# Kernel optimization log

Measured on AMD Instinct MI355X. Metric: run time of the kernel, lower is better.

## Reference

```python
import jax, jax.numpy as jnp
import numpy as np

N = 3072      # packed vision tokens (multiple of _BLOCK=128, so no padding needed)
D = 1280      # hidden_size
H = 16        # num_heads
K = 80        # head_dim = D // H
NSEG = 8      # number of packed images/segments


def setup_inputs() -> dict:
    key = jax.random.key(0)
    ks = jax.random.split(key, 8)
    hidden_ND = jax.random.normal(ks[0], (N, D), jnp.float32)
    inner = jnp.sort(jax.random.randint(ks[1], (NSEG - 1,), 1, N)).astype(jnp.int32)
    cu_seqlens = jnp.concatenate([
        jnp.zeros((1,), jnp.int32), inner, jnp.full((1,), N, jnp.int32)])
    theta = jax.random.uniform(ks[2], (N, K), jnp.float32, 0.0, 2.0 * np.pi)
    cos_NK = jnp.cos(theta)
    sin_NK = jnp.sin(theta)
    sd = 1.0 / np.sqrt(D)  # lecun_normal-ish scale
    qkv_w = jax.random.normal(ks[3], (D, 3 * D), jnp.float32) * sd
    qkv_b = jax.random.normal(ks[4], (3 * D,), jnp.float32) * 0.01
    proj_w = jax.random.normal(ks[5], (D, D), jnp.float32) * sd
    proj_b = jax.random.normal(ks[6], (D,), jnp.float32) * 0.01
    return {"hidden_ND": hidden_ND, "cu_seqlens": cu_seqlens,
            "cos_NK": cos_NK, "sin_NK": sin_NK,
            "qkv_w": qkv_w, "qkv_b": qkv_b,
            "proj_w": proj_w, "proj_b": proj_b}


def _rotate_half(x):
    x1, x2 = jnp.split(x, 2, axis=-1)
    return jnp.concatenate([-x2, x1], axis=-1)


def _apply_vision_rope(q_NHK, k_NHK, cos_NK, sin_NK):
    c = cos_NK[:, None, :]  # (N, 1, K) broadcast over heads
    s = sin_NK[:, None, :]
    q = q_NHK * c + _rotate_half(q_NHK) * s
    k = k_NHK * c + _rotate_half(k_NHK) * s
    return q, k


def reference(hidden_ND, cu_seqlens, cos_NK, sin_NK, qkv_w, qkv_b, proj_w, proj_b):
    n = hidden_ND.shape[0]
    scale = K ** (-0.5)
    qkv = (hidden_ND @ qkv_w + qkv_b).reshape(n, 3, H, K)
    q_NHK, k_NHK, v_NHK = qkv[:, 0], qkv[:, 1], qkv[:, 2]
    q_NHK, k_NHK = _apply_vision_rope(q_NHK, k_NHK, cos_NK, sin_NK)

    # segment-boundary mask: token i attends to [k_start[i], k_end[i])
    idx = jnp.arange(n)
    seg = jnp.searchsorted(cu_seqlens[1:], idx, side='right')
    nseg = cu_seqlens.shape[0]
    k_start = cu_seqlens[jnp.minimum(seg, nseg - 2)]
    k_end = cu_seqlens[jnp.minimum(seg + 1, nseg - 1)]
    mask = (idx[None, :] >= k_start[:, None]) & (idx[None, :] < k_end[:, None])  # (Nq, Nk)

    scores = jnp.einsum('nhk,mhk->hnm', q_NHK, k_NHK) * scale  # (H, N, N)
    scores = jnp.where(mask[None], scores, jnp.float32(-1e30))
    probs = jax.nn.softmax(scores, axis=-1)
    attn = jnp.einsum('hnm,mhk->nhk', probs, v_NHK)  # (N, H, K)
    out_ND = attn.reshape(n, H * K) @ proj_w + proj_b
    return out_ND
```

## Files before the change

kernel.cpp:

```cpp
#include <hip/hip_runtime.h>

#define NTOK 3072
#define DM   1280
#define NH   16
#define HD   80
#define HDS  104
#define KVB  64
#define NSEG 8
#define QKVC 3840

typedef __attribute__((ext_vector_type(4))) float  f32x4;
typedef __attribute__((ext_vector_type(8))) __bf16 bf16x8;
typedef __attribute__((ext_vector_type(8))) unsigned short ushort8;
typedef __attribute__((ext_vector_type(4))) unsigned short ushort4v;

static __device__ __forceinline__ unsigned short f2bf(float f){
  union{float f; unsigned int u;} v; v.f=f;
  unsigned int r = v.u + 0x7fffu + ((v.u>>16)&1u);
  return (unsigned short)(r>>16);
}
static __device__ __forceinline__ float bf2f(unsigned short u){
  union{unsigned int i; float f;} v; v.i = ((unsigned int)u)<<16; return v.f;
}
static __device__ __forceinline__ void gload_lds16(const void* g, void* l){
  __builtin_amdgcn_global_load_lds((const __attribute__((address_space(1))) void*)g,
                                   (__attribute__((address_space(3))) void*)l, 16, 0, 0);
}

__global__ void cast_f32_bf16(const float* __restrict__ src, unsigned short* __restrict__ dst, int n){
  int i = (blockIdx.x*256 + threadIdx.x)*4;
  if (i >= n) return;
  f32x4 v = *reinterpret_cast<const f32x4*>(&src[i]);
  ushort4v o;
  o[0]=f2bf(v[0]); o[1]=f2bf(v[1]); o[2]=f2bf(v[2]); o[3]=f2bf(v[3]);
  *reinterpret_cast<ushort4v*>(&dst[i]) = o;
}

__global__ void transpose_cast(const float* __restrict__ src, unsigned short* __restrict__ dst, int R, int C){
  __shared__ unsigned short tile[32][33];
  int c0 = blockIdx.x*32, r0 = blockIdx.y*32;
  int tx = threadIdx.x, ty = threadIdx.y;
  #pragma unroll
  for (int i=0;i<4;i++){
    int r = r0 + ty + i*8;
    tile[ty+i*8][tx] = f2bf(src[(size_t)r*C + c0 + tx]);
  }
  __syncthreads();
  #pragma unroll
  for (int i=0;i<4;i++){
    int c = c0 + ty + i*8;
    dst[(size_t)c*R + r0 + tx] = tile[tx][ty+i*8];
  }
}

__global__ void transpose_v(const unsigned short* __restrict__ qkv, unsigned short* __restrict__ Vt){
  __shared__ unsigned short tile[32][33];
  int n0 = blockIdx.x*32, d0 = blockIdx.y*32, h = blockIdx.z;
  int tx = threadIdx.x, ty = threadIdx.y;
  #pragma unroll
  for (int i=0;i<4;i++){
    int n = n0 + ty + i*8;
    int d = d0 + tx;
    tile[ty+i*8][tx] = (d < HD) ? qkv[(size_t)n*QKVC + 2*DM + h*HD + d] : (unsigned short)0;
  }
  __syncthreads();
  #pragma unroll
  for (int i=0;i<4;i++){
    int d = d0 + ty + i*8;
    if (d < HD) Vt[((size_t)h*HD + d)*NTOK + n0 + tx] = tile[tx][ty+i*8];
  }
}

template<int OUT_BF16>
__global__ __launch_bounds__(256) void gemm_bt(
    const unsigned short* __restrict__ A,
    const unsigned short* __restrict__ Bt,
    const float* __restrict__ bias,
    unsigned short* __restrict__ Cb,
    float* __restrict__ Cf,
    int M, int Ncol, int Kd)
{
  __shared__ unsigned short As[2][128*32];
  __shared__ unsigned short Bs[2][128*32];
  const int tid  = threadIdx.x;
  const int lane = tid & 63, wave = tid >> 6;
  const int wr = wave >> 1, wc = wave & 1;
  const int bm = blockIdx.y, bn = blockIdx.x;
  const f32x4 vzero = {0.f,0.f,0.f,0.f};

  f32x4 acc[4][4];
  #pragma unroll
  for (int i=0;i<4;i++)
    #pragma unroll
    for (int j=0;j<4;j++) acc[i][j] = vzero;

  const int rsub = lane>>2;
  const int kc   = (lane&3)*8;
  const unsigned short* Ab = A  + (size_t)(bm*128 + wave*32 + rsub)*Kd + kc;
  const unsigned short* Bb = Bt + (size_t)(bn*128 + wave*32 + rsub)*Kd + kc;

  #pragma unroll
  for (int i=0;i<2;i++){
    gload_lds16(Ab + (size_t)i*16*Kd, &As[0][(wave*2+i)*512]);
    gload_lds16(Bb + (size_t)i*16*Kd, &Bs[0][(wave*2+i)*512]);
  }
  __syncthreads();

  int cur = 0;
  for (int k0=32; k0<Kd; k0+=32){
    #pragma unroll
    for (int i=0;i<2;i++){
      gload_lds16(Ab + (size_t)i*16*Kd + k0, &As[cur^1][(wave*2+i)*512]);
      gload_lds16(Bb + (size_t)i*16*Kd + k0, &Bs[cur^1][(wave*2+i)*512]);
    }
    bf16x8 a[4], b[4];
    #pragma unroll
    for (int mf=0; mf<4; mf++)
      a[mf] = *reinterpret_cast<const bf16x8*>(&As[cur][(wr*64 + mf*16 + (lane&15))*32 + ((lane>>4)<<3)]);
    #pragma unroll
    for (int nf=0; nf<4; nf++)
      b[nf] = *reinterpret_cast<const bf16x8*>(&Bs[cur][(wc*64 + nf*16 + (lane&15))*32 + ((lane>>4)<<3)]);
    #pragma unroll
    for (int mf=0; mf<4; mf++)
      #pragma unroll
      for (int nf=0; nf<4; nf++)
        acc[mf][nf] = __builtin_amdgcn_mfma_f32_16x16x32_bf16(a[mf], b[nf], acc[mf][nf], 0,0,0);
    __syncthreads();
    cur ^= 1;
  }
  {
    bf16x8 a[4], b[4];
    #pragma unroll
    for (int mf=0; mf<4; mf++)
      a[mf] = *reinterpret_cast<const bf16x8*>(&As[cur][(wr*64 + mf*16 + (lane&15))*32 + ((lane>>4)<<3)]);
    #pragma unroll
    for (int nf=0; nf<4; nf++)
      b[nf] = *reinterpret_cast<const bf16x8*>(&Bs[cur][(wc*64 + nf*16 + (lane&15))*32 + ((lane>>4)<<3)]);
    #pragma unroll
    for (int mf=0; mf<4; mf++)
      #pragma unroll
      for (int nf=0; nf<4; nf++)
        acc[mf][nf] = __builtin_amdgcn_mfma_f32_16x16x32_bf16(a[mf], b[nf], acc[mf][nf], 0,0,0);
  }

  const int crow0 = bm*128 + wr*64;
  const int ccol0 = bn*128 + wc*64;
  #pragma unroll
  for (int nf=0; nf<4; nf++){
    int col = ccol0 + nf*16 + (lane&15);
    float bv = bias[col];
    #pragma unroll
    for (int mf=0; mf<4; mf++){
      #pragma unroll
      for (int r=0;r<4;r++){
        int row = crow0 + mf*16 + ((lane>>4)<<2) + r;
        float v = acc[mf][nf][r] + bv;
        if (OUT_BF16) Cb[(size_t)row*Ncol + col] = f2bf(v);
        else          Cf[(size_t)row*Ncol + col] = v;
      }
    }
  }
}

__global__ void rope_repack(const unsigned short* __restrict__ qkv,
                            const float* __restrict__ cosNK, const float* __restrict__ sinNK,
                            unsigned short* __restrict__ Qr, unsigned short* __restrict__ Kr)
{
  int idx = blockIdx.x*256 + threadIdx.x;
  if (idx >= NH*NTOK*HDS) return;
  int k  = idx % HDS;
  int nh = idx / HDS;
  int n  = nh % NTOK;
  int h  = nh / NTOK;
  size_t dsti = (size_t)(h*NTOK + n)*HDS + k;
  if (k >= HD){ Qr[dsti]=0; Kr[dsti]=0; return; }
  float c = cosNK[n*HD + k], s = sinNK[n*HD + k];
  int   kp  = (k < 40) ? (k+40) : (k-40);
  float sgn = (k < 40) ? -1.f : 1.f;
  size_t base = (size_t)n*QKVC + h*HD;
  float q   = bf2f(qkv[base + k]);
  float qp  = bf2f(qkv[base + kp]);
  float kk  = bf2f(qkv[base + DM + k]);
  float kkp = bf2f(qkv[base + DM + kp]);
  Qr[dsti] = f2bf(q*c  + sgn*qp*s);
  Kr[dsti] = f2bf(kk*c + sgn*kkp*s);
}

__global__ __launch_bounds__(256) void attn_kernel(
    const unsigned short* __restrict__ Qr,
    const unsigned short* __restrict__ Kr,
    const unsigned short* __restrict__ Vt,
    const int* __restrict__ cu,
    unsigned short* __restrict__ attn_out)
{
  __shared__ unsigned short Qs[64*HDS];
  __shared__ unsigned short Ks[2][KVB*HDS];
  __shared__ unsigned short Ps[64*KVB];
  __shared__ int rs[64], re[64];

  const int h   = blockIdx.y;
  const int q0  = blockIdx.x*64;
  const int tid = threadIdx.x;
  const int lane = tid & 63, wave = tid >> 6;
  const int l16 = lane & 15, g16 = lane >> 4;
  const f32x4 vzero = {0.f,0.f,0.f,0.f};

  if (tid < 64){
    int row = q0 + tid, seg = 0;
    #pragma unroll
    for (int j=1;j<NSEG;j++) seg += (cu[j] <= row) ? 1 : 0;
    rs[tid] = cu[seg]; re[tid] = cu[seg+1];
  }
  int seg0 = 0, seg1 = 0;
  #pragma unroll
  for (int j=1;j<NSEG;j++){
    seg0 += (cu[j] <= q0) ? 1 : 0;
    seg1 += (cu[j] <= q0+63) ? 1 : 0;
  }
  const int kmin = cu[seg0], kmax = cu[seg1+1];
  const int kt0 = kmin & ~(KVB-1);
  const int nt  = (kmax - kt0 + KVB-1)/KVB;

  {
    const char* src = (const char*)(Qr + (size_t)(h*NTOK + q0)*HDS);
    #pragma unroll
    for (int i=0;i<4;i++){
      int t = tid + i*256;
      if (t < 832) gload_lds16(src + (size_t)t*16, (char*)Qs + (size_t)t*16);
    }
  }
  {
    const char* src = (const char*)(Kr + (size_t)(h*NTOK + kt0)*HDS);
    #pragma unroll
    for (int i=0;i<4;i++){
      int t = tid + i*256;
      if (t < 832) gload_lds16(src + (size_t)t*16, (char*)Ks[0] + (size_t)t*16);
    }
  }
  __syncthreads();

  f32x4 accO[5];
  #pragma unroll
  for (int i=0;i<5;i++) accO[i] = vzero;
  float m_r[4] = {-1e30f,-1e30f,-1e30f,-1e30f};
  float l_r[4] = {0.f,0.f,0.f,0.f};
  const float scale = 0.11180339887498948f;

  int cur = 0;
  for (int it = 0; it < nt; ++it){
    const int kt  = kt0 + it*KVB;
    const int ktn = kt0 + ((it+1 < nt) ? (it+1) : (nt-1))*KVB;
    {
      const char* src = (const char*)(Kr + (size_t)(h*NTOK + ktn)*HDS);
      #pragma unroll
      for (int i=0;i<4;i++){
        int t = tid + i*256;
        if (t < 832) gload_lds16(src + (size_t)t*16, (char*)Ks[cur^1] + (size_t)t*16);
      }
    }
    ushort8 vreg[2][5];
    #pragma unroll
    for (int ks=0; ks<2; ks++)
      #pragma unroll
      for (int cf=0; cf<5; cf++)
        vreg[ks][cf] = *reinterpret_cast<const ushort8*>(
            &Vt[((size_t)h*HD + cf*16 + l16)*NTOK + kt + ks*32 + g16*8]);

    f32x4 accS[4];
    #pragma unroll
    for (int i=0;i<4;i++) accS[i] = vzero;
    #pragma unroll
    for (int ks=0; ks<3; ks++){
      bf16x8 aq = *reinterpret_cast<const bf16x8*>((const char*)Qs + (wave*16 + l16)*208 + ks*64 + g16*16);
      #pragma unroll
      for (int nf=0;nf<4;nf++){
        bf16x8 bk = *reinterpret_cast<const bf16x8*>((const char*)Ks[cur] + (nf*16 + l16)*208 + ks*64 + g16*16);
        accS[nf] = __builtin_amdgcn_mfma_f32_16x16x32_bf16(aq, bk, accS[nf], 0,0,0);
      }
    }
    #pragma unroll
    for (int r=0;r<4;r++){
      const int row_i = wave*16 + g16*4 + r;
      const int rst = rs[row_i], ren = re[row_i];
      float sv[4]; bool ok[4];
      float mx = -1e30f;
      #pragma unroll
      for (int nf=0;nf<4;nf++){
        int kcol = kt + nf*16 + l16;
        ok[nf] = (kcol >= rst) && (kcol < ren);
        sv[nf] = accS[nf][r]*scale;
        if (ok[nf]) mx = fmaxf(mx, sv[nf]);
      }
      #pragma unroll
      for (int d=1; d<16; d<<=1) mx = fmaxf(mx, __shfl_xor(mx, d, 64));
      float mnew  = fmaxf(m_r[r], mx);
      float alpha = __expf(m_r[r] - mnew);
      m_r[r] = mnew;
      float lsum = 0.f;
      #pragma unroll
      for (int nf=0;nf<4;nf++){
        float p = ok[nf] ? __expf(sv[nf] - mnew) : 0.f;
        int pb = (row_i*128 + nf*32 + l16*2) ^ ((row_i&7)<<4);
        *reinterpret_cast<unsigned short*>((char*)Ps + pb) = f2bf(p);
        lsum += p;
      }
      #pragma unroll
      for (int d=1; d<16; d<<=1) lsum += __shfl_xor(lsum, d, 64);
      l_r[r] = l_r[r]*alpha + lsum;
      #pragma unroll
      for (int cf=0; cf<5; cf++) accO[cf][r] *= alpha;
    }
    #pragma unroll
    for (int ks=0; ks<2; ks++){
      const int arow = wave*16 + l16;
      bf16x8 ap = *reinterpret_cast<const bf16x8*>((char*)Ps + ((arow*128 + ks*64 + g16*16) ^ ((arow&7)<<4)));
      #pragma unroll
      for (int cf=0; cf<5; cf++){
        bf16x8 bv = __builtin_bit_cast(bf16x8, vreg[ks][cf]);
        accO[cf] = __builtin_amdgcn_mfma_f32_16x16x32_bf16(ap, bv, accO[cf], 0,0,0);
      }
    }
    __syncthreads();
    cur ^= 1;
  }

  #pragma unroll
  for (int cf=0; cf<5; cf++){
    #pragma unroll
    for (int r=0;r<4;r++){
      int row = q0 + wave*16 + g16*4 + r;
      int col = h*HD + cf*16 + l16;
      attn_out[(size_t)row*DM + col] = f2bf(accO[cf][r] / l_r[r]);
    }
  }
}

extern "C" void kernel_launch(void* const* d_in, const int* in_sizes, int n_in,
                              void* d_out, int out_size, void* d_ws, size_t ws_size,
                              hipStream_t stream)
{
  const float* hidden = (const float*)d_in[0];
  const int*   cu     = (const int*)  d_in[1];
  const float* cosNK  = (const float*)d_in[2];
  const float* sinNK  = (const float*)d_in[3];
  const float* qkv_w  = (const float*)d_in[4];
  const float* qkv_b  = (const float*)d_in[5];
  const float* proj_w = (const float*)d_in[6];
  const float* proj_b = (const float*)d_in[7];
  float* out = (float*)d_out;

  char* w = (char*)d_ws;
  unsigned short* hid_bf  = (unsigned short*)w;  w += (size_t)NTOK*DM*2;
  unsigned short* qkvwT   = (unsigned short*)w;  w += (size_t)QKVC*DM*2;
  unsigned short* projwT  = (unsigned short*)w;  w += (size_t)DM*DM*2;
  unsigned short* qkv_bf  = (unsigned short*)w;  w += (size_t)NTOK*QKVC*2;
  unsigned short* Qr      = (unsigned short*)w;  w += (size_t)NH*NTOK*HDS*2;
  unsigned short* Kr      = (unsigned short*)w;  w += (size_t)NH*NTOK*HDS*2;
  unsigned short* Vt      = qkvwT;
  unsigned short* attn_bf = hid_bf;

  cast_f32_bf16<<<(NTOK*DM/4 + 255)/256, 256, 0, stream>>>(hidden, hid_bf, NTOK*DM);
  transpose_cast<<<dim3(QKVC/32, DM/32), dim3(32,8), 0, stream>>>(qkv_w, qkvwT, DM, QKVC);
  transpose_cast<<<dim3(DM/32,  DM/32), dim3(32,8), 0, stream>>>(proj_w, projwT, DM, DM);
  gemm_bt<1><<<dim3(QKVC/128, NTOK/128), 256, 0, stream>>>(hid_bf, qkvwT, qkv_b, qkv_bf, nullptr, NTOK, QKVC, DM);
  rope_repack<<<(NH*NTOK*HDS + 255)/256, 256, 0, stream>>>(qkv_bf, cosNK, sinNK, Qr, Kr);
  transpose_v<<<dim3(NTOK/32, 3, NH), dim3(32,8), 0, stream>>>(qkv_bf, Vt);
  attn_kernel<<<dim3(NTOK/64, NH), 256, 0, stream>>>(Qr, Kr, Vt, cu, attn_bf);
  gemm_bt<0><<<dim3(DM/128, NTOK/128), 256, 0, stream>>>(attn_bf, projwT, proj_b, nullptr, out, NTOK, DM, DM);
}
```

Baseline: 268.2 us.

## Compute transposed S in attention with Q in registers; remap GEMM blocks across XCDs

The attention kernel now computes S transposed (K·Q^T), so each lane owns one query row. Q stays in registers, K is read straight from global memory instead of being staged in LDS, and the per-row max and sum reductions drop to two shuffles. This removes the LDS staging and the __syncthreads barrier, and lets the output be written as vector stores. Both GEMMs switch to a 1-D grid whose block ids are remapped by id mod 8, intended to give each XCD a contiguous group of output tiles for better L2 reuse; the cost is that K loads no longer go through LDS and get no reuse there.

```diff
diff --git a/kernel.cpp b/kernel.cpp
--- a/kernel.cpp
+++ b/kernel.cpp
@@ -13,6 +13,7 @@
 typedef __attribute__((ext_vector_type(8))) __bf16 bf16x8;
 typedef __attribute__((ext_vector_type(8))) unsigned short ushort8;
 typedef __attribute__((ext_vector_type(4))) unsigned short ushort4v;
+typedef __attribute__((ext_vector_type(2))) unsigned int  u32x2;
 
 static __device__ __forceinline__ unsigned short f2bf(float f){
   union{float f; unsigned int u;} v; v.f=f;
@@ -78,14 +79,16 @@
     const float* __restrict__ bias,
     unsigned short* __restrict__ Cb,
     float* __restrict__ Cf,
-    int M, int Ncol, int Kd)
+    int M, int Ncol, int Kd, int nbn)
 {
   __shared__ unsigned short As[2][128*32];
   __shared__ unsigned short Bs[2][128*32];
   const int tid  = threadIdx.x;
   const int lane = tid & 63, wave = tid >> 6;
   const int wr = wave >> 1, wc = wave & 1;
-  const int bm = blockIdx.y, bn = blockIdx.x;
+  const int cpx = gridDim.x >> 3;
+  const int id  = (blockIdx.x & 7)*cpx + (blockIdx.x >> 3);
+  const int bm = id / nbn, bn = id % nbn;
   const f32x4 vzero = {0.f,0.f,0.f,0.f};
 
   f32x4 acc[4][4];
@@ -193,71 +196,47 @@
     const int* __restrict__ cu,
     unsigned short* __restrict__ attn_out)
 {
-  __shared__ unsigned short Qs[64*HDS];
-  __shared__ unsigned short Ks[2][KVB*HDS];
   __shared__ unsigned short Ps[64*KVB];
-  __shared__ int rs[64], re[64];
 
   const int h   = blockIdx.y;
   const int q0  = blockIdx.x*64;
   const int tid = threadIdx.x;
   const int lane = tid & 63, wave = tid >> 6;
   const int l16 = lane & 15, g16 = lane >> 4;
+  const int qrow = q0 + wave*16 + l16;
   const f32x4 vzero = {0.f,0.f,0.f,0.f};
 
-  if (tid < 64){
-    int row = q0 + tid, seg = 0;
-    #pragma unroll
-    for (int j=1;j<NSEG;j++) seg += (cu[j] <= row) ? 1 : 0;
-    rs[tid] = cu[seg]; re[tid] = cu[seg+1];
-  }
-  int seg0 = 0, seg1 = 0;
+  int seg = 0, seg0 = 0, seg1 = 0;
   #pragma unroll
   for (int j=1;j<NSEG;j++){
-    seg0 += (cu[j] <= q0) ? 1 : 0;
-    seg1 += (cu[j] <= q0+63) ? 1 : 0;
-  }
+    int c = cu[j];
+    seg  += (c <= qrow)  ? 1 : 0;
+    seg0 += (c <= q0)    ? 1 : 0;
+    seg1 += (c <= q0+63) ? 1 : 0;
+  }
+  const int rst = cu[seg], ren = cu[seg+1];
   const int kmin = cu[seg0], kmax = cu[seg1+1];
   const int kt0 = kmin & ~(KVB-1);
-  const int nt  = (kmax - kt0 + KVB-1)/KVB;
-
+
+  bf16x8 bq[3];
   {
-    const char* src = (const char*)(Qr + (size_t)(h*NTOK + q0)*HDS);
-    #pragma unroll
-    for (int i=0;i<4;i++){
-      int t = tid + i*256;
-      if (t < 832) gload_lds16(src + (size_t)t*16, (char*)Qs + (size_t)t*16);
-    }
-  }
-  {
-    const char* src = (const char*)(Kr + (size_t)(h*NTOK + kt0)*HDS);
-    #pragma unroll
-    for (int i=0;i<4;i++){
-      int t = tid + i*256;
-      if (t < 832) gload_lds16(src + (size_t)t*16, (char*)Ks[0] + (size_t)t*16);
-    }
-  }
-  __syncthreads();
+    const unsigned short* qsrc = Qr + ((size_t)h*NTOK + qrow)*HDS;
+    #pragma unroll
+    for (int ds=0; ds<3; ds++)
+      bq[ds] = *reinterpret_cast<const bf16x8*>(&qsrc[ds*32 + g16*8]);
+  }
 
   f32x4 accO[5];
   #pragma unroll
   for (int i=0;i<5;i++) accO[i] = vzero;
-  float m_r[4] = {-1e30f,-1e30f,-1e30f,-1e30f};
-  float l_r[4] = {0.f,0.f,0.f,0.f};
+  float m_r = -1e30f, l_r = 0.f;
   const float scale = 0.11180339887498948f;
 
-  int cur = 0;
-  for (int it = 0; it < nt; ++it){
-    const int kt  = kt0 + it*KVB;
-    const int ktn = kt0 + ((it+1 < nt) ? (it+1) : (nt-1))*KVB;
-    {
-      const char* src = (const char*)(Kr + (size_t)(h*NTOK + ktn)*HDS);
-      #pragma unroll
-      for (int i=0;i<4;i++){
-        int t = tid + i*256;
-        if (t < 832) gload_lds16(src + (size_t)t*16, (char*)Ks[cur^1] + (size_t)t*16);
-      }
-    }
+  const int prow  = wave*16 + l16;
+  char* const psb = (char*)Ps;
+  const int pswz  = (prow & 7) << 4;
+
+  for (int kt = kt0; kt < kmax; kt += KVB){
     ushort8 vreg[2][5];
     #pragma unroll
     for (int ks=0; ks<2; ks++)
@@ -266,72 +245,78 @@
         vreg[ks][cf] = *reinterpret_cast<const ushort8*>(
             &Vt[((size_t)h*HD + cf*16 + l16)*NTOK + kt + ks*32 + g16*8]);
 
-    f32x4 accS[4];
-    #pragma unroll
-    for (int i=0;i<4;i++) accS[i] = vzero;
-    #pragma unroll
-    for (int ks=0; ks<3; ks++){
-      bf16x8 aq = *reinterpret_cast<const bf16x8*>((const char*)Qs + (wave*16 + l16)*208 + ks*64 + g16*16);
-      #pragma unroll
-      for (int nf=0;nf<4;nf++){
-        bf16x8 bk = *reinterpret_cast<const bf16x8*>((const char*)Ks[cur] + (nf*16 + l16)*208 + ks*64 + g16*16);
-        accS[nf] = __builtin_amdgcn_mfma_f32_16x16x32_bf16(aq, bk, accS[nf], 0,0,0);
-      }
-    }
-    #pragma unroll
-    for (int r=0;r<4;r++){
-      const int row_i = wave*16 + g16*4 + r;
-      const int rst = rs[row_i], ren = re[row_i];
-      float sv[4]; bool ok[4];
-      float mx = -1e30f;
-      #pragma unroll
-      for (int nf=0;nf<4;nf++){
-        int kcol = kt + nf*16 + l16;
-        ok[nf] = (kcol >= rst) && (kcol < ren);
-        sv[nf] = accS[nf][r]*scale;
-        if (ok[nf]) mx = fmaxf(mx, sv[nf]);
-      }
-      #pragma unroll
-      for (int d=1; d<16; d<<=1) mx = fmaxf(mx, __shfl_xor(mx, d, 64));
-      float mnew  = fmaxf(m_r[r], mx);
-      float alpha = __expf(m_r[r] - mnew);
-      m_r[r] = mnew;
-      float lsum = 0.f;
-      #pragma unroll
-      for (int nf=0;nf<4;nf++){
-        float p = ok[nf] ? __expf(sv[nf] - mnew) : 0.f;
-        int pb = (row_i*128 + nf*32 + l16*2) ^ ((row_i&7)<<4);
-        *reinterpret_cast<unsigned short*>((char*)Ps + pb) = f2bf(p);
-        lsum += p;
-      }
-      #pragma unroll
-      for (int d=1; d<16; d<<=1) lsum += __shfl_xor(lsum, d, 64);
-      l_r[r] = l_r[r]*alpha + lsum;
-      #pragma unroll
-      for (int cf=0; cf<5; cf++) accO[cf][r] *= alpha;
-    }
+    const unsigned short* ksrc = Kr + ((size_t)h*NTOK + kt)*HDS;
+    f32x4 accST[4];
+    #pragma unroll
+    for (int i=0;i<4;i++) accST[i] = vzero;
+    #pragma unroll
+    for (int ds=0; ds<3; ds++){
+      #pragma unroll
+      for (int f=0; f<4; f++){
+        bf16x8 ak = *reinterpret_cast<const bf16x8*>(&ksrc[(size_t)(f*16 + l16)*HDS + ds*32 + g16*8]);
+        accST[f] = __builtin_amdgcn_mfma_f32_16x16x32_bf16(ak, bq[ds], accST[f], 0,0,0);
+      }
+    }
+
+    float mx = -1e30f;
+    #pragma unroll
+    for (int f=0; f<4; f++){
+      #pragma unroll
+      for (int r=0; r<4; r++){
+        int kcol = kt + f*16 + g16*4 + r;
+        bool ok = (kcol >= rst) && (kcol < ren);
+        float s = accST[f][r]*scale;
+        accST[f][r] = ok ? s : -3e38f;
+        mx = fmaxf(mx, accST[f][r]);
+      }
+    }
+    mx = fmaxf(mx, __shfl_xor(mx, 16));
+    mx = fmaxf(mx, __shfl_xor(mx, 32));
+    const float mnew  = fmaxf(m_r, mx);
+    const float alpha = __expf(m_r - mnew);
+    m_r = mnew;
+    float lsum = 0.f;
+    #pragma unroll
+    for (int f=0; f<4; f++){
+      #pragma unroll
+      for (int r=0; r<4; r++){
+        float e = __expf(accST[f][r] - mnew);
+        accST[f][r] = e;
+        lsum += e;
+      }
+    }
+    lsum += __shfl_xor(lsum, 16);
+    lsum += __shfl_xor(lsum, 32);
+    l_r = l_r*alpha + lsum;
+    #pragma unroll
+    for (int cf=0; cf<5; cf++) accO[cf] *= alpha;
+
+    #pragma unroll
+    for (int f=0; f<4; f++){
+      u32x2 pk;
+      pk[0] = (unsigned int)f2bf(accST[f][0]) | ((unsigned int)f2bf(accST[f][1]) << 16);
+      pk[1] = (unsigned int)f2bf(accST[f][2]) | ((unsigned int)f2bf(accST[f][3]) << 16);
+      *reinterpret_cast<u32x2*>(psb + ((prow*128 + f*32 + g16*8) ^ pswz)) = pk;
+    }
+
     #pragma unroll
     for (int ks=0; ks<2; ks++){
-      const int arow = wave*16 + l16;
-      bf16x8 ap = *reinterpret_cast<const bf16x8*>((char*)Ps + ((arow*128 + ks*64 + g16*16) ^ ((arow&7)<<4)));
+      bf16x8 bp = *reinterpret_cast<const bf16x8*>(psb + ((prow*128 + ks*64 + g16*16) ^ pswz));
       #pragma unroll
       for (int cf=0; cf<5; cf++){
-        bf16x8 bv = __builtin_bit_cast(bf16x8, vreg[ks][cf]);
-        accO[cf] = __builtin_amdgcn_mfma_f32_16x16x32_bf16(ap, bv, accO[cf], 0,0,0);
-      }
-    }
-    __syncthreads();
-    cur ^= 1;
-  }
-
+        bf16x8 av = __builtin_bit_cast(bf16x8, vreg[ks][cf]);
+        accO[cf] = __builtin_amdgcn_mfma_f32_16x16x32_bf16(av, bp, accO[cf], 0,0,0);
+      }
+    }
+  }
+
+  const float inv = 1.f / l_r;
   #pragma unroll
   for (int cf=0; cf<5; cf++){
-    #pragma unroll
-    for (int r=0;r<4;r++){
-      int row = q0 + wave*16 + g16*4 + r;
-      int col = h*HD + cf*16 + l16;
-      attn_out[(size_t)row*DM + col] = f2bf(accO[cf][r] / l_r[r]);
-    }
+    ushort4v o;
+    #pragma unroll
+    for (int r=0;r<4;r++) o[r] = f2bf(accO[cf][r]*inv);
+    *reinterpret_cast<ushort4v*>(&attn_out[(size_t)qrow*DM + h*HD + cf*16 + g16*4]) = o;
   }
 }
 
@@ -362,9 +347,9 @@
   cast_f32_bf16<<<(NTOK*DM/4 + 255)/256, 256, 0, stream>>>(hidden, hid_bf, NTOK*DM);
   transpose_cast<<<dim3(QKVC/32, DM/32), dim3(32,8), 0, stream>>>(qkv_w, qkvwT, DM, QKVC);
   transpose_cast<<<dim3(DM/32,  DM/32), dim3(32,8), 0, stream>>>(proj_w, projwT, DM, DM);
-  gemm_bt<1><<<dim3(QKVC/128, NTOK/128), 256, 0, stream>>>(hid_bf, qkvwT, qkv_b, qkv_bf, nullptr, NTOK, QKVC, DM);
+  gemm_bt<1><<<dim3((NTOK/128)*(QKVC/128)), 256, 0, stream>>>(hid_bf, qkvwT, qkv_b, qkv_bf, nullptr, NTOK, QKVC, DM, QKVC/128);
   rope_repack<<<(NH*NTOK*HDS + 255)/256, 256, 0, stream>>>(qkv_bf, cosNK, sinNK, Qr, Kr);
   transpose_v<<<dim3(NTOK/32, 3, NH), dim3(32,8), 0, stream>>>(qkv_bf, Vt);
   attn_kernel<<<dim3(NTOK/64, NH), 256, 0, stream>>>(Qr, Kr, Vt, cu, attn_bf);
-  gemm_bt<0><<<dim3(DM/128, NTOK/128), 256, 0, stream>>>(attn_bf, projwT, proj_b, nullptr, out, NTOK, DM, DM);
-}
+  gemm_bt<0><<<dim3((NTOK/128)*(DM/128)), 256, 0, stream>>>(attn_bf, projwT, proj_b, nullptr, out, NTOK, DM, DM, DM/128);
+}
```

After: 256.3 us. 1.05x faster.
